# Performance work log

Hardware: AMD Instinct MI355X
Metric: run time of the kernel (lower is better)

Reference implementation:

```python
import jax, jax.numpy as jnp
import numpy as np

T = 3000
D_MODEL = 1280
NUM_HEADS = 20
HEAD_DIM = D_MODEL // NUM_HEADS
N_CHUNKS = 4  # block-diagonal chunks of 750 frames each
NEG = -1e9


def _block_diag_mask(t, n_chunks):
    chunk = t // n_chunks
    seg = jnp.arange(t) // chunk  # [T]
    allow = seg[:, None] == seg[None, :]
    return jnp.where(allow, 0.0, NEG).astype(jnp.float32)


def setup_inputs() -> dict:
    key = jax.random.key(0)
    ks = jax.random.split(key, 9)
    s = 1.0 / np.sqrt(D_MODEL)
    inp = {
        "hidden_states": jax.random.normal(ks[0], (T, D_MODEL), jnp.float32),
        "attention_mask": _block_diag_mask(T, N_CHUNKS),
        "wq": jax.random.normal(ks[1], (D_MODEL, D_MODEL), jnp.float32) * s,
        "bq": jax.random.normal(ks[2], (D_MODEL,), jnp.float32) * 0.02,
        "wk": jax.random.normal(ks[3], (D_MODEL, D_MODEL), jnp.float32) * s,
        "bk": jax.random.normal(ks[4], (D_MODEL,), jnp.float32) * 0.02,
        "wv": jax.random.normal(ks[5], (D_MODEL, D_MODEL), jnp.float32) * s,
        "bv": jax.random.normal(ks[6], (D_MODEL,), jnp.float32) * 0.02,
        "wo": jax.random.normal(ks[7], (D_MODEL, D_MODEL), jnp.float32) * s,
        "bo": jax.random.normal(ks[8], (D_MODEL,), jnp.float32) * 0.02,
    }
    return inp


def reference(hidden_states, attention_mask, wq, bq, wk, bk, wv, bv, wo, bo):
    # hidden_states: [T, D], attention_mask: [T, T] additive (0 / -inf)
    t = hidden_states.shape[0]
    scaling = HEAD_DIM ** -0.5
    # projections -> [H, T, hd]  (weights stored as [in, out] = W^T of nn.Linear)
    q = (hidden_states @ wq + bq).reshape(t, NUM_HEADS, HEAD_DIM).transpose(1, 0, 2)
    k = (hidden_states @ wk + bk).reshape(t, NUM_HEADS, HEAD_DIM).transpose(1, 0, 2)
    v = (hidden_states @ wv + bv).reshape(t, NUM_HEADS, HEAD_DIM).transpose(1, 0, 2)
    # [H, T, T] scores + additive mask, fp32 softmax
    scores = jnp.einsum("htd,hsd->hts", q, k) * scaling + attention_mask[None]
    attn = jax.nn.softmax(scores.astype(jnp.float32), axis=-1).astype(q.dtype)
    out = jnp.einsum("hts,hsd->htd", attn, v)  # [H, T, hd]
    out = out.transpose(1, 0, 2).reshape(t, D_MODEL)
    return out @ wo + bo
```

## Files before the change

### kernel.cpp

```cpp
#include <hip/hip_runtime.h>

#define T_LEN 3000
#define DM 1280
#define NUM_HEADS 20
#define N_CH 4
#define CHUNK 750
#define CHUNK_PAD 768
#define T_PAD 3072

typedef __bf16 bf16x8 __attribute__((ext_vector_type(8)));
typedef float f32x4 __attribute__((ext_vector_type(4)));

typedef const __attribute__((address_space(1))) void* gas_p;
typedef __attribute__((address_space(3))) void* las_p;
#define GLOAD16(g, l) __builtin_amdgcn_global_load_lds((gas_p)(g), (las_p)(l), 16, 0, 0)

__device__ __forceinline__ unsigned short f2bf(float f) {
  union { float f; unsigned u; } x; x.f = f;
  unsigned r = x.u + 0x7FFFu + ((x.u >> 16) & 1u);
  return (unsigned short)(r >> 16);
}

__global__ __launch_bounds__(256) void cvt_bf16_kernel(
    const float* __restrict__ in, unsigned short* __restrict__ out) {
  int i = blockIdx.x * 256 + threadIdx.x;
  ushort4 o;
  if (i < T_LEN * DM / 4) {
    const float4 v = ((const float4*)in)[i];
    o.x = f2bf(v.x); o.y = f2bf(v.y); o.z = f2bf(v.z); o.w = f2bf(v.w);
  } else {
    o.x = 0; o.y = 0; o.z = 0; o.w = 0;
  }
  ((ushort4*)out)[i] = o;
}

__global__ __launch_bounds__(256) void tr_bf16_kernel(
    const float* __restrict__ w0, const float* __restrict__ w1,
    const float* __restrict__ w2, const float* __restrict__ w3,
    unsigned short* __restrict__ out) {
  const int z = blockIdx.z;
  const float* in = z == 0 ? w0 : (z == 1 ? w1 : (z == 2 ? w2 : w3));
  unsigned short* o = out + (size_t)z * DM * DM;
  __shared__ float tile[32][33];
  const int x = threadIdx.x, y0 = threadIdx.y;
  const int n0 = blockIdx.x * 32, k0 = blockIdx.y * 32;
  for (int y = y0; y < 32; y += 8) tile[y][x] = in[(k0 + y) * DM + n0 + x];
  __syncthreads();
  for (int y = y0; y < 32; y += 8) o[(n0 + y) * DM + k0 + x] = f2bf(tile[x][y]);
}

__global__ __launch_bounds__(256) void vpad_zero_kernel(unsigned short* __restrict__ Vtb) {
  int i = blockIdx.x * 256 + threadIdx.x;
  if (i >= NUM_HEADS * 64 * N_CH * (CHUNK_PAD - CHUNK)) return;
  int c = i % (CHUNK_PAD - CHUNK); int r = i / (CHUNK_PAD - CHUNK);
  int ch = r % N_CH; int row = r / N_CH;
  Vtb[(size_t)row * T_PAD + ch * CHUNK_PAD + CHUNK + c] = 0;
}

template <int MODE>
__global__ __launch_bounds__(256) void gemm_kernel(
    const unsigned short* __restrict__ A, const unsigned short* __restrict__ Bt,
    const float* __restrict__ b0, const float* __restrict__ b1, const float* __restrict__ b2,
    unsigned short* __restrict__ dq, unsigned short* __restrict__ dk,
    unsigned short* __restrict__ dv, float* __restrict__ df) {
  __shared__ unsigned short As[128][64];
  __shared__ unsigned short Bs[128][64];
  const int tid = threadIdx.x;
  const int lane = tid & 63, wave = tid >> 6;
  const int h = lane >> 4, lr = lane & 15;
  const int wm = wave >> 1, wn = wave & 1;
  const int t0 = blockIdx.x * 128, n0 = blockIdx.y * 128;
  const int rs = lane >> 3;
  const int c8 = (lane & 7) ^ rs;

  const unsigned short* Ab = A + (size_t)t0 * DM + c8 * 8;
  const unsigned short* Bb = Bt + (size_t)n0 * DM + c8 * 8;

  f32x4 acc[4][4];
  const f32x4 zero4 = {0.f, 0.f, 0.f, 0.f};
#pragma unroll
  for (int i = 0; i < 4; i++)
#pragma unroll
    for (int j = 0; j < 4; j++) acc[i][j] = zero4;

  const int NT = DM / 64;
  for (int kt = 0; kt < NT; ++kt) {
    const int k0 = kt * 64;
#pragma unroll
    for (int i = 0; i < 4; ++i) {
      const int blk = wave * 4 + i;
      const size_t ro = (size_t)(blk * 8 + rs) * DM + k0;
      GLOAD16(Ab + ro, &As[blk * 8][0]);
      GLOAD16(Bb + ro, &Bs[blk * 8][0]);
    }
    __syncthreads();
#pragma unroll
    for (int kk = 0; kk < 2; ++kk) {
      bf16x8 a[4], b[4];
      const int csw = ((kk * 4 + h) ^ (lr & 7)) * 8;
#pragma unroll
      for (int mi = 0; mi < 4; mi++) a[mi] = *(const bf16x8*)&As[wm * 64 + mi * 16 + lr][csw];
#pragma unroll
      for (int ni = 0; ni < 4; ni++) b[ni] = *(const bf16x8*)&Bs[wn * 64 + ni * 16 + lr][csw];
#pragma unroll
      for (int mi = 0; mi < 4; mi++)
#pragma unroll
        for (int ni = 0; ni < 4; ni++)
          acc[mi][ni] = __builtin_amdgcn_mfma_f32_16x16x32_bf16(a[mi], b[ni], acc[mi][ni], 0, 0, 0);
    }
    __syncthreads();
  }

  const int sec = (MODE == 0) ? (blockIdx.y / 10) : 0;
  const float* bias = (MODE == 0) ? (sec == 0 ? b0 : (sec == 1 ? b1 : b2)) : b0;
  const float qs = (MODE == 0 && sec == 0) ? 0.125f : 1.0f;
#pragma unroll
  for (int mi = 0; mi < 4; mi++) {
#pragma unroll
    for (int j = 0; j < 4; j++) {
      int t = t0 + wm * 64 + mi * 16 + h * 4 + j;
      if (t >= T_LEN) continue;
#pragma unroll
      for (int ni = 0; ni < 4; ni++) {
        int n = n0 + wn * 64 + ni * 16 + lr;
        if (MODE == 0) {
          int nn = n - sec * DM;
          float v = (acc[mi][ni][j] + bias[nn]) * qs;
          if (sec < 2) {
            unsigned short* dst = sec == 0 ? dq : dk;
            dst[(size_t)(nn >> 6) * (T_PAD * 64) + (size_t)t * 64 + (nn & 63)] = f2bf(v);
          } else {
            int ch = t / CHUNK, s = t - ch * CHUNK;
            dv[(size_t)(nn >> 6) * (64 * T_PAD) + (size_t)(nn & 63) * T_PAD + ch * CHUNK_PAD + s] = f2bf(v);
          }
        } else {
          df[(size_t)t * DM + n] = acc[mi][ni][j] + bias[n];
        }
      }
    }
  }
}

__global__ __launch_bounds__(256) void attn_kernel(
    const unsigned short* __restrict__ Qb, const unsigned short* __restrict__ Kb,
    const unsigned short* __restrict__ Vtb, unsigned short* __restrict__ Ctx) {
  __shared__ unsigned short Ks[2][64][64];
  __shared__ unsigned short Vs[2][64][64];
  __shared__ unsigned short Ps[4][16][64];
  const int tid = threadIdx.x;
  const int lane = tid & 63, wave = tid >> 6;
  const int h = lane >> 4, lr = lane & 15;
  const int rs = lane >> 3;
  const int c8 = (lane & 7) ^ rs;
  int bid = blockIdx.x;
  const int qt = bid % 12; bid /= 12;
  const int ch = bid % N_CH; bid /= N_CH;
  const int hh = bid;

  const unsigned short* Qh = Qb + (size_t)hh * (T_PAD * 64);
  const unsigned short* Kh = Kb + (size_t)hh * (T_PAD * 64) + (size_t)(ch * CHUNK) * 64 + c8 * 8;
  const unsigned short* Vh = Vtb + (size_t)hh * (64 * T_PAD) + ch * CHUNK_PAD + c8 * 8;

  const int qrow0 = qt * 64 + wave * 16;
  const int tq = ch * CHUNK + qrow0 + lr;
  bf16x8 aq[2];
#pragma unroll
  for (int kk = 0; kk < 2; kk++)
    aq[kk] = *(const bf16x8*)(Qh + (size_t)tq * 64 + kk * 32 + h * 8);

  const f32x4 zero4 = {0.f, 0.f, 0.f, 0.f};
  f32x4 oacc[4];
#pragma unroll
  for (int i = 0; i < 4; i++) oacc[i] = zero4;
  float l_part[4] = {0.f, 0.f, 0.f, 0.f};

#define A_STAGE(buf, kt) do {                                                   \
    const int s0_ = (kt) * 64;                                                  \
    _Pragma("unroll")                                                           \
    for (int i_ = 0; i_ < 2; ++i_) {                                            \
      const int blk_ = wave * 2 + i_;                                           \
      const int r_ = blk_ * 8 + rs;                                             \
      GLOAD16(Kh + (size_t)(s0_ + r_) * 64, &Ks[buf][blk_ * 8][0]);             \
      GLOAD16(Vh + (size_t)r_ * T_PAD + s0_, &Vs[buf][blk_ * 8][0]);            \
    } } while (0)

  A_STAGE(0, 0);
  __syncthreads();
  int cur = 0;
  for (int kt = 0; kt < 12; ++kt) {
    if (kt + 1 < 12) A_STAGE(cur ^ 1, kt + 1);

    f32x4 sacc[4];
#pragma unroll
    for (int i = 0; i < 4; i++) sacc[i] = zero4;
#pragma unroll
    for (int kk = 0; kk < 2; kk++) {
      const int csw = ((kk * 4 + h) ^ (lr & 7)) * 8;
      bf16x8 bk[4];
#pragma unroll
      for (int ni = 0; ni < 4; ni++) bk[ni] = *(const bf16x8*)&Ks[cur][ni * 16 + lr][csw];
#pragma unroll
      for (int ni = 0; ni < 4; ni++)
        sacc[ni] = __builtin_amdgcn_mfma_f32_16x16x32_bf16(aq[kk], bk[ni], sacc[ni], 0, 0, 0);
    }

    const bool last = (kt == 11);
    float pexp[4][4];
#pragma unroll
    for (int ni = 0; ni < 4; ni++) {
#pragma unroll
      for (int j = 0; j < 4; j++) {
        float e = __expf(sacc[ni][j]);
        if (last && (ni * 16 + lr >= CHUNK - 704)) e = 0.f;
        pexp[ni][j] = e;
        l_part[j] += e;
      }
    }

#pragma unroll
    for (int ni = 0; ni < 4; ni++) {
#pragma unroll
      for (int j = 0; j < 4; j++) {
        int row = h * 4 + j;
        int col = ni * 16 + lr;
        Ps[wave][row][((col >> 3) ^ (row & 7)) * 8 + (col & 7)] = f2bf(pexp[ni][j]);
      }
    }

#pragma unroll
    for (int kk = 0; kk < 2; kk++) {
      const int csw = ((kk * 4 + h) ^ (lr & 7)) * 8;
      bf16x8 ap = *(const bf16x8*)&Ps[wave][lr][csw];
      bf16x8 bv[4];
#pragma unroll
      for (int nd = 0; nd < 4; nd++) bv[nd] = *(const bf16x8*)&Vs[cur][nd * 16 + lr][csw];
#pragma unroll
      for (int nd = 0; nd < 4; nd++)
        oacc[nd] = __builtin_amdgcn_mfma_f32_16x16x32_bf16(ap, bv[nd], oacc[nd], 0, 0, 0);
    }
    __syncthreads();
    cur ^= 1;
  }
#undef A_STAGE

#pragma unroll
  for (int j = 0; j < 4; j++) {
    float l = l_part[j];
#pragma unroll
    for (int off = 1; off < 16; off <<= 1) l += __shfl_xor(l, off, 64);
    int qr = qrow0 + h * 4 + j;
    if (qr >= CHUNK) continue;
    int t = ch * CHUNK + qr;
    float inv = 1.f / l;
#pragma unroll
    for (int nd = 0; nd < 4; nd++) {
      int d = nd * 16 + lr;
      Ctx[(size_t)t * DM + hh * 64 + d] = f2bf(oacc[nd][j] * inv);
    }
  }
}

extern "C" void kernel_launch(void* const* d_in, const int* in_sizes, int n_in,
                              void* d_out, int out_size, void* d_ws, size_t ws_size,
                              hipStream_t stream) {
  const float* hs = (const float*)d_in[0];
  const float* wq = (const float*)d_in[2];
  const float* bq = (const float*)d_in[3];
  const float* wk = (const float*)d_in[4];
  const float* bk = (const float*)d_in[5];
  const float* wv = (const float*)d_in[6];
  const float* bv = (const float*)d_in[7];
  const float* wo = (const float*)d_in[8];
  const float* bo = (const float*)d_in[9];

  char* ws = (char*)d_ws;
  unsigned short* Xb = (unsigned short*)ws;   ws += (size_t)T_PAD * DM * 2;
  unsigned short* Wcat = (unsigned short*)ws; ws += (size_t)4 * DM * DM * 2;
  unsigned short* Qb = (unsigned short*)ws;   ws += (size_t)NUM_HEADS * T_PAD * 64 * 2;
  unsigned short* Kb = (unsigned short*)ws;   ws += (size_t)NUM_HEADS * T_PAD * 64 * 2;
  unsigned short* Vtb = (unsigned short*)ws;  ws += (size_t)NUM_HEADS * 64 * T_PAD * 2;
  unsigned short* Ctx = (unsigned short*)ws;  ws += (size_t)T_PAD * DM * 2;

  cvt_bf16_kernel<<<T_PAD * DM / 4 / 256, 256, 0, stream>>>(hs, Xb);
  tr_bf16_kernel<<<dim3(40, 40, 4), dim3(32, 8), 0, stream>>>(wq, wk, wv, wo, Wcat);
  vpad_zero_kernel<<<(NUM_HEADS * 64 * N_CH * (CHUNK_PAD - CHUNK) + 255) / 256, 256, 0, stream>>>(Vtb);

  gemm_kernel<0><<<dim3(24, 30), 256, 0, stream>>>(Xb, Wcat, bq, bk, bv, Qb, Kb, Vtb, nullptr);

  attn_kernel<<<NUM_HEADS * N_CH * 12, 256, 0, stream>>>(Qb, Kb, Vtb, Ctx);

  gemm_kernel<1><<<dim3(24, 10), 256, 0, stream>>>(Ctx, Wcat + (size_t)3 * DM * DM, bo, nullptr, nullptr,
                                                   nullptr, nullptr, nullptr, (float*)d_out);
}
```

Baseline: 133.1 us.

## Triple-buffer GEMM K-loop with async LDS loads and remap block order

Rewrites the projection GEMM main loop to use a 3-stage LDS ring with 32-wide K tiles. Global-to-LDS loads for step k+2 are issued while MFMAs run on step k, using vmcnt waits plus a single barrier per step instead of two syncthreads. It also launches a 1D grid with a swizzled block-to-tile mapping, which is meant to improve L2 reuse across XCDs. The cost is more LDS per block, smaller K tiles, and fragile manual waitcnt logic.

```diff
diff --git a/kernel.cpp b/kernel.cpp
--- a/kernel.cpp
+++ b/kernel.cpp
@@ -63,18 +63,27 @@
     const float* __restrict__ b0, const float* __restrict__ b1, const float* __restrict__ b2,
     unsigned short* __restrict__ dq, unsigned short* __restrict__ dk,
     unsigned short* __restrict__ dv, float* __restrict__ df) {
-  __shared__ unsigned short As[128][64];
-  __shared__ unsigned short Bs[128][64];
+  __shared__ unsigned short As[3][128 * 32];
+  __shared__ unsigned short Bs[3][128 * 32];
   const int tid = threadIdx.x;
   const int lane = tid & 63, wave = tid >> 6;
   const int h = lane >> 4, lr = lane & 15;
   const int wm = wave >> 1, wn = wave & 1;
-  const int t0 = blockIdx.x * 128, n0 = blockIdx.y * 128;
-  const int rs = lane >> 3;
-  const int c8 = (lane & 7) ^ rs;
-
-  const unsigned short* Ab = A + (size_t)t0 * DM + c8 * 8;
-  const unsigned short* Bb = Bt + (size_t)n0 * DM + c8 * 8;
+
+  const int NB = (MODE == 0) ? 720 : 240;
+  const int GY = (MODE == 0) ? 30 : 10;
+  const int swz = (blockIdx.x & 7) * (NB / 8) + (blockIdx.x >> 3);
+  const int bx = swz / GY, by = swz % GY;
+  const int t0 = bx * 128, n0 = by * 128;
+
+  const int srow = lane >> 2;
+  const int c4 = lane & 3;
+  const int r0 = wave * 32 + srow;
+  const int r1 = r0 + 16;
+  const unsigned short* a0p = A + (size_t)(t0 + r0) * DM + ((c4 ^ ((r0 >> 1) & 3)) * 8);
+  const unsigned short* a1p = A + (size_t)(t0 + r1) * DM + ((c4 ^ ((r1 >> 1) & 3)) * 8);
+  const unsigned short* b0p = Bt + (size_t)(n0 + r0) * DM + ((c4 ^ ((r0 >> 1) & 3)) * 8);
+  const unsigned short* b1p = Bt + (size_t)(n0 + r1) * DM + ((c4 ^ ((r1 >> 1) & 3)) * 8);
 
   f32x4 acc[4][4];
   const f32x4 zero4 = {0.f, 0.f, 0.f, 0.f};
@@ -83,35 +92,58 @@
 #pragma unroll
     for (int j = 0; j < 4; j++) acc[i][j] = zero4;
 
-  const int NT = DM / 64;
-  for (int kt = 0; kt < NT; ++kt) {
-    const int k0 = kt * 64;
-#pragma unroll
-    for (int i = 0; i < 4; ++i) {
-      const int blk = wave * 4 + i;
-      const size_t ro = (size_t)(blk * 8 + rs) * DM + k0;
-      GLOAD16(Ab + ro, &As[blk * 8][0]);
-      GLOAD16(Bb + ro, &Bs[blk * 8][0]);
-    }
-    __syncthreads();
-#pragma unroll
-    for (int kk = 0; kk < 2; ++kk) {
-      bf16x8 a[4], b[4];
-      const int csw = ((kk * 4 + h) ^ (lr & 7)) * 8;
-#pragma unroll
-      for (int mi = 0; mi < 4; mi++) a[mi] = *(const bf16x8*)&As[wm * 64 + mi * 16 + lr][csw];
-#pragma unroll
-      for (int ni = 0; ni < 4; ni++) b[ni] = *(const bf16x8*)&Bs[wn * 64 + ni * 16 + lr][csw];
-#pragma unroll
-      for (int mi = 0; mi < 4; mi++)
-#pragma unroll
-        for (int ni = 0; ni < 4; ni++)
-          acc[mi][ni] = __builtin_amdgcn_mfma_f32_16x16x32_bf16(a[mi], b[ni], acc[mi][ni], 0, 0, 0);
-    }
-    __syncthreads();
-  }
-
-  const int sec = (MODE == 0) ? (blockIdx.y / 10) : 0;
+#define G_STAGE(SP, kt) do {                                         \
+    const size_t ko_ = (size_t)(kt) * 32;                            \
+    GLOAD16(a0p + ko_, &As[SP][(wave * 32) * 32]);                   \
+    GLOAD16(a1p + ko_, &As[SP][(wave * 32 + 16) * 32]);              \
+    GLOAD16(b0p + ko_, &Bs[SP][(wave * 32) * 32]);                   \
+    GLOAD16(b1p + ko_, &Bs[SP][(wave * 32 + 16) * 32]);              \
+  } while (0)
+
+  const int NT = DM / 32;
+
+#define K_STEP(kt, SL, SP) do {                                                \
+    if ((kt) + 2 < NT) G_STAGE(SP, (kt) + 2);                                  \
+    bf16x8 a[4], b[4];                                                         \
+    _Pragma("unroll")                                                          \
+    for (int mi = 0; mi < 4; mi++) {                                           \
+      const int row = wm * 64 + mi * 16 + lr;                                  \
+      a[mi] = *(const bf16x8*)&As[SL][row * 32 + (h ^ ((row >> 1) & 3)) * 8];  \
+    }                                                                          \
+    _Pragma("unroll")                                                          \
+    for (int ni = 0; ni < 4; ni++) {                                           \
+      const int col = wn * 64 + ni * 16 + lr;                                  \
+      b[ni] = *(const bf16x8*)&Bs[SL][col * 32 + (h ^ ((col >> 1) & 3)) * 8];  \
+    }                                                                          \
+    _Pragma("unroll")                                                          \
+    for (int mi = 0; mi < 4; mi++)                                             \
+      _Pragma("unroll")                                                        \
+      for (int ni = 0; ni < 4; ni++)                                           \
+        acc[mi][ni] = __builtin_amdgcn_mfma_f32_16x16x32_bf16(a[mi], b[ni], acc[mi][ni], 0, 0, 0); \
+    if ((kt) + 1 < NT) {                                                       \
+      if ((kt) + 2 < NT) { asm volatile("s_waitcnt vmcnt(4)" ::: "memory"); }  \
+      else               { asm volatile("s_waitcnt vmcnt(0)" ::: "memory"); }  \
+      __builtin_amdgcn_s_barrier();                                            \
+      asm volatile("" ::: "memory");                                           \
+    }                                                                          \
+  } while (0)
+
+  G_STAGE(0, 0);
+  G_STAGE(1, 1);
+  asm volatile("s_waitcnt vmcnt(4)" ::: "memory");
+  __builtin_amdgcn_s_barrier();
+  asm volatile("" ::: "memory");
+
+  for (int kt = 0; kt < NT - 1; kt += 3) {
+    K_STEP(kt, 0, 2);
+    K_STEP(kt + 1, 1, 0);
+    K_STEP(kt + 2, 2, 1);
+  }
+  K_STEP(NT - 1, 0, 2);
+#undef K_STEP
+#undef G_STAGE
+
+  const int sec = (MODE == 0) ? (by / 10) : 0;
   const float* bias = (MODE == 0) ? (sec == 0 ? b0 : (sec == 1 ? b1 : b2)) : b0;
   const float qs = (MODE == 0 && sec == 0) ? 0.125f : 1.0f;
 #pragma unroll
@@ -285,10 +317,10 @@
   tr_bf16_kernel<<<dim3(40, 40, 4), dim3(32, 8), 0, stream>>>(wq, wk, wv, wo, Wcat);
   vpad_zero_kernel<<<(NUM_HEADS * 64 * N_CH * (CHUNK_PAD - CHUNK) + 255) / 256, 256, 0, stream>>>(Vtb);
 
-  gemm_kernel<0><<<dim3(24, 30), 256, 0, stream>>>(Xb, Wcat, bq, bk, bv, Qb, Kb, Vtb, nullptr);
+  gemm_kernel<0><<<720, 256, 0, stream>>>(Xb, Wcat, bq, bk, bv, Qb, Kb, Vtb, nullptr);
 
   attn_kernel<<<NUM_HEADS * N_CH * 12, 256, 0, stream>>>(Qb, Kb, Vtb, Ctx);
 
-  gemm_kernel<1><<<dim3(24, 10), 256, 0, stream>>>(Ctx, Wcat + (size_t)3 * DM * DM, bo, nullptr, nullptr,
-                                                   nullptr, nullptr, nullptr, (float*)d_out);
-}
+  gemm_kernel<1><<<240, 256, 0, stream>>>(Ctx, Wcat + (size_t)3 * DM * DM, bo, nullptr, nullptr,
+                                          nullptr, nullptr, nullptr, (float*)d_out);
+}
```

Measured after the change: 181.8 us. 1.37x slower.
